# Kernel optimization log

Measured on AMD Instinct MI355X. Metric: run time of the kernel, lower is better.

Reference implementation:

```python
import jax, jax.numpy as jnp
import numpy as np

BS, Q, S1, S2 = 8, 128, 32, 64
H_DIM, NH = 768, 12
DH = H_DIM // NH


def _linear_params(k, scale=0.02):
    kw, _ = jax.random.split(k)
    w = jax.random.normal(kw, (H_DIM, H_DIM), jnp.float32) * scale
    b = jnp.zeros((H_DIM,), jnp.float32)
    return w, b


def setup_inputs() -> dict:
    root = jax.random.key(0)
    ks = jax.random.split(root, 12)
    wq_w, wq_b = _linear_params(ks[0])
    wk_w, wk_b = _linear_params(ks[1])
    wv_w, wv_b = _linear_params(ks[2])
    sq_w, sq_b = _linear_params(ks[3])
    sk_w, sk_b = _linear_params(ks[4])
    sv_w, sv_b = _linear_params(ks[5])
    return {
        "q_in": jax.random.normal(ks[6], (BS, Q, H_DIM), jnp.float32),
        "k_in": jax.random.normal(ks[7], (BS, S1, S2, H_DIM), jnp.float32),
        "v_in": jax.random.normal(ks[8], (BS, S1, S2, H_DIM), jnp.float32),
        "kvec": jax.random.normal(ks[9], (BS, S1, H_DIM), jnp.float32),
        "word_mask": jnp.ones((BS, S1, S2), jnp.int32),
        "sentence_mask": jnp.ones((BS * Q, S1), jnp.int32),
        "wq_w": wq_w, "wq_b": wq_b, "wk_w": wk_w, "wk_b": wk_b,
        "wv_w": wv_w, "wv_b": wv_b, "sq_w": sq_w, "sq_b": sq_b,
        "sk_w": sk_w, "sk_b": sk_b, "sv_w": sv_w, "sv_b": sv_b,
    }


def reference(q_in, k_in, v_in, kvec, word_mask, sentence_mask,
              wq_w, wq_b, wk_w, wk_b, wv_w, wv_b,
              sq_w, sq_b, sk_w, sk_b, sv_w, sv_b):
    bs, q_len = q_in.shape[0], q_in.shape[1]
    s1, s2 = k_in.shape[1], k_in.shape[2]
    scale = 1.0 / jnp.sqrt(jnp.float32(DH))

    # additive masks, as in the torch module
    wm = (1.0 - word_mask.astype(jnp.float32)) * -10000.0      # [bs, s1, s2]
    sm = (1.0 - sentence_mask.astype(jnp.float32)) * -10000.0  # [bs*Q, s1]

    # ---- word-level attention ----
    q = (q_in @ wq_w + wq_b).reshape(bs, q_len, NH, DH)
    k = (k_in @ wk_w + wk_b).reshape(bs, s1, s2, NH, DH)
    v = (v_in @ wv_w + wv_b).reshape(bs, s1, s2, NH, DH)
    # scores over tokens within each sentence: [bs, s1, H, Q, s2]
    scores1 = jnp.einsum('bqhd,bsthd->bshqt', q, k) * scale
    probs1 = jax.nn.softmax(scores1 + wm[:, :, None, None, :], axis=-1)
    # word_hidden: [bs, Q, s1, h]
    wh = jnp.einsum('bshqt,bsthd->bqshd', probs1, v).reshape(bs, q_len, s1, H_DIM)

    # ---- sentence-level attention ----
    sq = (q_in @ sq_w + sq_b).reshape(bs, q_len, NH, DH)
    sk = (kvec @ sk_w + sk_b).reshape(bs, s1, NH, DH)   # shared across queries
    sv = (wh @ sv_w + sv_b).reshape(bs, q_len, s1, NH, DH)
    scores2 = jnp.einsum('bqhd,bshd->bqhs', sq, sk) * scale  # [bs, Q, H, s1]
    scores2 = scores2 + sm.reshape(bs, q_len, s1)[:, :, None, :]
    probs2 = jax.nn.softmax(scores2, axis=-1)
    out = jnp.einsum('bqhs,bqshd->bqhd', probs2, sv).reshape(bs * q_len, H_DIM)
    return out
```

## Files before the change

kernel.cpp:

```cpp
#include <hip/hip_runtime.h>
#include <hip/hip_bf16.h>


typedef __attribute__((ext_vector_type(8))) short short8;
typedef __attribute__((ext_vector_type(4))) short short4v;
typedef __attribute__((ext_vector_type(4))) float f32x4;

__device__ __forceinline__ short f2bf(float f) {
  __hip_bfloat16 b = __float2bfloat16(f);
  return __builtin_bit_cast(short, b);
}
__device__ __forceinline__ float bf2f(short s) {
  __hip_bfloat16 b = __builtin_bit_cast(__hip_bfloat16, s);
  return __bfloat162float(b);
}

#define MFMA16(a, b, c) __builtin_amdgcn_mfma_f32_16x16x32_bf16((a), (b), (c), 0, 0, 0)

__device__ __forceinline__ void async_load16(const void* g, void* l) {
  auto l3 = (__attribute__((address_space(3))) void*)(uintptr_t)(
      reinterpret_cast<uintptr_t>(l));
  auto g1 = (const __attribute__((address_space(1))) void*)g;
  __builtin_amdgcn_global_load_lds(g1, l3, 16, 0, 0);
}

__global__ __launch_bounds__(256)
void prep(const float* __restrict__ w0, const float* __restrict__ w1,
          const float* __restrict__ w2, const float* __restrict__ w3,
          const float* __restrict__ w4, const float* __restrict__ w5,
          short* __restrict__ WT,
          const float* __restrict__ q_in, const float* __restrict__ k_in,
          const float* __restrict__ v_in, const float* __restrict__ kvec,
          short* __restrict__ qbf, short* __restrict__ kbf,
          short* __restrict__ vbf, short* __restrict__ kvb) {
  const int id = blockIdx.x;
  const int tid = threadIdx.x;
  if (id < 3456) {
    __shared__ float tile[32][33];
    const int zz = id / 576, r = id % 576;
    const float* W = (zz == 0) ? w0 : (zz == 1) ? w1 : (zz == 2) ? w2
                   : (zz == 3) ? w3 : (zz == 4) ? w4 : w5;
    short* WTo = WT + (size_t)zz * 768 * 768;
    const int bx = (r % 24) * 32, by = (r / 24) * 32;
    const int tx = tid & 31, ty = tid >> 5;
    #pragma unroll
    for (int i = 0; i < 32; i += 8)
      tile[ty + i][tx] = W[(size_t)(by + ty + i) * 768 + bx + tx];
    __syncthreads();
    #pragma unroll
    for (int i = 0; i < 32; i += 8)
      WTo[(size_t)(bx + ty + i) * 768 + by + tx] = f2bf(tile[tx][ty + i]);
    return;
  }
  const int i = (id - 3456) * 256 + tid;
  const float* src;
  short* dst;
  int idx;
  if (i < 98304)        { src = q_in; dst = qbf; idx = i; }
  else if (i < 1671168) { src = k_in; dst = kbf; idx = i - 98304; }
  else if (i < 3244032) { src = v_in; dst = vbf; idx = i - 1671168; }
  else                  { src = kvec; dst = kvb; idx = i - 3244032; }
  const float4* s = (const float4*)src + (size_t)idx * 2;
  const float4 a = s[0], b = s[1];
  __align__(16) short tmp[8] = {f2bf(a.x), f2bf(a.y), f2bf(a.z), f2bf(a.w),
                                f2bf(b.x), f2bf(b.y), f2bf(b.z), f2bf(b.w)};
  *((short8*)dst + idx) = *(short8*)tmp;
}

template<int OUT_MODE>
__global__ __launch_bounds__(256)
void gemm(const short* __restrict__ Ap, const short* __restrict__ Ap2,
          const short* __restrict__ WTa, const short* __restrict__ WTb,
          const float* __restrict__ bias_a, const float* __restrict__ bias_b,
          const float* __restrict__ probs2, void* __restrict__ Outp,
          void* __restrict__ Outp2) {
  const int K = 768;
  __shared__ __align__(16) short As[128 * 32];
  __shared__ __align__(16) short Bs[128 * 32];
  const int z = (OUT_MODE == 5) ? blockIdx.z : 0;
  const short* A = (OUT_MODE == 5 && z) ? Ap2 : Ap;
  const short* WT = (OUT_MODE == 5 && z) ? WTb : WTa;
  const float* bias = (OUT_MODE == 5 && z) ? bias_b : bias_a;

  const int tid = threadIdx.x;
  const int m0 = blockIdx.x * 128, n0 = blockIdx.y * 128;
  const int w = tid >> 6, lane = tid & 63, quad = lane >> 4, l16 = lane & 15;
  const int wm = (w >> 1) * 64, wn = (w & 1) * 64;

  const int grow = w * 32 + (lane >> 2);
  const int kc = (lane & 3) * 8;
  const short* ag = A + (size_t)(m0 + grow) * K + kc;
  const short* bg = WT + (size_t)(n0 + grow) * K + kc;
  short* al = &As[(w * 32) * 32];
  short* bl = &Bs[(w * 32) * 32];

  const f32x4 zero4 = {0.f, 0.f, 0.f, 0.f};
  f32x4 acc[4][4];
  #pragma unroll
  for (int i = 0; i < 4; i++)
    #pragma unroll
    for (int j = 0; j < 4; j++) acc[i][j] = zero4;

  for (int k0 = 0; k0 < K; k0 += 32) {
    __syncthreads();
    async_load16(ag, al);
    async_load16(ag + (size_t)16 * K, al + 16 * 32);
    async_load16(bg, bl);
    async_load16(bg + (size_t)16 * K, bl + 16 * 32);
    ag += 32;
    bg += 32;
    __syncthreads();
    short8 af[4], bf[4];
    #pragma unroll
    for (int i = 0; i < 4; i++)
      af[i] = *(short8*)&As[(wm + i * 16 + l16) * 32 + quad * 8];
    #pragma unroll
    for (int j = 0; j < 4; j++)
      bf[j] = *(short8*)&Bs[(wn + j * 16 + l16) * 32 + quad * 8];
    #pragma unroll
    for (int i = 0; i < 4; i++)
      #pragma unroll
      for (int j = 0; j < 4; j++)
        acc[i][j] = MFMA16(af[i], bf[j], acc[i][j]);
  }

  if (OUT_MODE == 4) {
    const int h = (n0 + wn) >> 6;
    const int bq0 = (m0 + wm) >> 5;
    float p2[2][2][4];
    #pragma unroll
    for (int g2 = 0; g2 < 2; g2++)
      #pragma unroll
      for (int par = 0; par < 2; par++)
        #pragma unroll
        for (int r = 0; r < 4; r++)
          p2[g2][par][r] =
              probs2[((size_t)(bq0 + g2) * 12 + h) * 32 + par * 16 + quad * 4 + r];
    float red[4][2];
    #pragma unroll
    for (int j = 0; j < 4; j++)
      #pragma unroll
      for (int g2 = 0; g2 < 2; g2++) {
        float ps = 0.f;
        #pragma unroll
        for (int par = 0; par < 2; par++)
          #pragma unroll
          for (int r = 0; r < 4; r++)
            ps += p2[g2][par][r] * acc[g2 * 2 + par][j][r];
        ps += __shfl_xor(ps, 16);
        ps += __shfl_xor(ps, 32);
        red[j][g2] = ps;
      }
    const int col = n0 + wn + quad * 16 + l16;
    const float bv = bias[col];
    float* outp = (float*)Outp;
    #pragma unroll
    for (int g2 = 0; g2 < 2; g2++)
      outp[(size_t)(bq0 + g2) * 768 + col] = red[quad][g2] + bv;
    return;
  }

  if (OUT_MODE == 5 && z == 1) {
    const int bs_ = (m0 + wm) >> 6;
    const int hh = (n0 + wn) >> 6;
    short* vT = (short*)Outp2;
    #pragma unroll
    for (int i = 0; i < 4; i++) {
      const int t0 = i * 16 + quad * 4;
      #pragma unroll
      for (int j = 0; j < 4; j++) {
        const int dd = j * 16 + l16;
        const float bv = bias[hh * 64 + dd];
        __align__(8) short tmp[4];
        #pragma unroll
        for (int r = 0; r < 4; r++) tmp[r] = f2bf(acc[i][j][r] + bv);
        *(short4v*)&vT[(((size_t)bs_ * 12 + hh) * 64 + dd) * 64 + t0] = *(short4v*)tmp;
      }
    }
    return;
  }

  #pragma unroll
  for (int i = 0; i < 4; i++) {
    #pragma unroll
    for (int j = 0; j < 4; j++) {
      const int col = n0 + wn + j * 16 + l16;
      float bv;
      if (OUT_MODE == 3)
        bv = (col < 768) ? bias_a[col] : bias_b[col - 768];
      else
        bv = bias[col];
      #pragma unroll
      for (int r = 0; r < 4; r++) {
        const int g = m0 + wm + i * 16 + quad * 4 + r;
        const float v = acc[i][j][r] + bv;
        if (OUT_MODE == 0) {
          ((float*)Outp)[(size_t)g * 768 + col] = v;
        } else if (OUT_MODE == 5) {
          ((short*)Outp)[(size_t)g * 768 + col] = f2bf(v);
        } else {
          if (col < 768)
            ((short*)Outp)[(size_t)g * 768 + col] = f2bf(v * 0.125f);
          else
            ((float*)Outp2)[(size_t)g * 768 + (col - 768)] = v;
        }
      }
    }
  }
}

__global__ __launch_bounds__(256)
void wattn_sp(const short* __restrict__ q_proj, const short* __restrict__ k_proj,
              const short* __restrict__ vT, const int* __restrict__ word_mask,
              const float* __restrict__ sq, const float* __restrict__ sk,
              const int* __restrict__ sent_mask, short* __restrict__ wh,
              float* __restrict__ probs2) {
  __shared__ __align__(16) short KVs[128 * 72];
  __shared__ __align__(16) short Ps[128 * 72];
  const int bid = blockIdx.x;
  const int tid = threadIdx.x;

  if (bid >= 3072) {
    float* sc = (float*)KVs;
    const int bq = bid - 3072;
    const int b = bq >> 7, q = bq & 127;
    for (int p = tid; p < 384; p += 256) {
      const int hh = p >> 5, ss = p & 31;
      const float4* a = (const float4*)(sq + ((size_t)(b * 128 + q)) * 768 + hh * 64);
      const float4* c = (const float4*)(sk + ((size_t)(b * 32 + ss)) * 768 + hh * 64);
      float d = 0.f;
      #pragma unroll
      for (int i = 0; i < 16; i++) {
        const float4 av = a[i], cv = c[i];
        d += av.x * cv.x + av.y * cv.y + av.z * cv.z + av.w * cv.w;
      }
      d = d * 0.125f + (1.0f - (float)sent_mask[bq * 32 + ss]) * -10000.0f;
      sc[hh * 33 + ss] = d;
    }
    __syncthreads();
    if (tid < 12) {
      float mx = -3.0e38f;
      for (int ss = 0; ss < 32; ss++) mx = fmaxf(mx, sc[tid * 33 + ss]);
      float sum = 0.f;
      for (int ss = 0; ss < 32; ss++) {
        const float e = __expf(sc[tid * 33 + ss] - mx);
        sc[tid * 33 + ss] = e;
        sum += e;
      }
      const float inv = 1.0f / sum;
      for (int ss = 0; ss < 32; ss++) sc[tid * 33 + ss] *= inv;
    }
    __syncthreads();
    for (int p = tid; p < 384; p += 256) {
      const int hh = p >> 5, ss = p & 31;
      probs2[((size_t)bq * 12 + hh) * 32 + ss] = sc[hh * 33 + ss];
    }
    return;
  }

  short* Ks = KVs;
  short* Vs = KVs + 64 * 72;
  short* Os = KVs;
  const int h = bid % 12, s = (bid / 12) % 32, b = bid / (12 * 32);
  const int w = tid >> 6, lane = tid & 63, quad = lane >> 4, l16 = lane & 15;
  const f32x4 zero4 = {0.f, 0.f, 0.f, 0.f};

  {
    const int t2 = tid & 127;
    const int row8 = t2 >> 3;
    const int c8 = (t2 & 7) * 8;
    if (tid < 128) {
      const short* src = k_proj + ((size_t)((b * 32 + s) * 64)) * 768 + h * 64 + c8;
      #pragma unroll
      for (int i = 0; i < 4; i++) {
        const int r = row8 + i * 16;
        *(short8*)&Ks[r * 72 + c8] = *(const short8*)(src + (size_t)r * 768);
      }
    } else {
      const short* src = vT + ((size_t)((b * 32 + s) * 12 + h)) * 4096 + c8;
      #pragma unroll
      for (int i = 0; i < 4; i++) {
        const int r = row8 + i * 16;
        *(short8*)&Vs[r * 72 + c8] = *(const short8*)(src + (size_t)r * 64);
      }
    }
  }
  __syncthreads();

  f32x4 sac[2][4];
  #pragma unroll
  for (int i = 0; i < 2; i++)
    #pragma unroll
    for (int j = 0; j < 4; j++) sac[i][j] = zero4;
  {
    short8 aq[2][2], bk[4][2];
    #pragma unroll
    for (int i = 0; i < 2; i++)
      #pragma unroll
      for (int kb = 0; kb < 2; kb++)
        aq[i][kb] = *(const short8*)(q_proj +
            ((size_t)(b * 128 + w * 32 + i * 16 + l16)) * 768 + h * 64 + kb * 32 + quad * 8);
    #pragma unroll
    for (int j = 0; j < 4; j++)
      #pragma unroll
      for (int kb = 0; kb < 2; kb++)
        bk[j][kb] = *(short8*)&Ks[(j * 16 + l16) * 72 + kb * 32 + quad * 8];
    #pragma unroll
    for (int i = 0; i < 2; i++)
      #pragma unroll
      for (int j = 0; j < 4; j++) {
        sac[i][j] = MFMA16(aq[i][0], bk[j][0], sac[i][j]);
        sac[i][j] = MFMA16(aq[i][1], bk[j][1], sac[i][j]);
      }
  }

  {
    float wmv[4];
    const int* wmp = word_mask + (b * 32 + s) * 64;
    #pragma unroll
    for (int j = 0; j < 4; j++)
      wmv[j] = (1.0f - (float)wmp[j * 16 + l16]) * -10000.0f;
    #pragma unroll
    for (int i = 0; i < 2; i++) {
      #pragma unroll
      for (int r = 0; r < 4; r++) {
        float vv[4];
        float sum = 0.f;
        #pragma unroll
        for (int j = 0; j < 4; j++) {
          vv[j] = __expf(sac[i][j][r] + wmv[j]);
          sum += vv[j];
        }
        sum += __shfl_xor(sum, 1);
        sum += __shfl_xor(sum, 2);
        sum += __shfl_xor(sum, 4);
        sum += __shfl_xor(sum, 8);
        const float inv = 1.0f / sum;
        const int row = w * 32 + i * 16 + quad * 4 + r;
        #pragma unroll
        for (int j = 0; j < 4; j++)
          Ps[row * 72 + j * 16 + l16] = f2bf(vv[j] * inv);
      }
    }
  }
  __syncthreads();

  f32x4 oac[2][4];
  #pragma unroll
  for (int i = 0; i < 2; i++)
    #pragma unroll
    for (int j = 0; j < 4; j++) oac[i][j] = zero4;
  {
    short8 ap[2][2], bv[4][2];
    #pragma unroll
    for (int i = 0; i < 2; i++)
      #pragma unroll
      for (int kb = 0; kb < 2; kb++)
        ap[i][kb] = *(short8*)&Ps[(w * 32 + i * 16 + l16) * 72 + kb * 32 + quad * 8];
    #pragma unroll
    for (int j = 0; j < 4; j++)
      #pragma unroll
      for (int kb = 0; kb < 2; kb++)
        bv[j][kb] = *(short8*)&Vs[(j * 16 + l16) * 72 + kb * 32 + quad * 8];
    #pragma unroll
    for (int i = 0; i < 2; i++)
      #pragma unroll
      for (int j = 0; j < 4; j++) {
        oac[i][j] = MFMA16(ap[i][0], bv[j][0], oac[i][j]);
        oac[i][j] = MFMA16(ap[i][1], bv[j][1], oac[i][j]);
      }
  }
  __syncthreads();
  #pragma unroll
  for (int i = 0; i < 2; i++)
    #pragma unroll
    for (int j = 0; j < 4; j++)
      #pragma unroll
      for (int r = 0; r < 4; r++)
        Os[(w * 32 + i * 16 + quad * 4 + r) * 72 + j * 16 + l16] = f2bf(oac[i][j][r]);
  __syncthreads();

  {
    const int c8 = (tid & 7) * 8;
    #pragma unroll
    for (int i = 0; i < 4; i++) {
      const int row = i * 32 + (tid >> 3);
      short* dst = wh + (((size_t)(b * 128 + row)) * 32 + s) * 768 + h * 64;
      *(short8*)(dst + c8) = *(const short8*)&Os[row * 72 + c8];
    }
  }
}

extern "C" void kernel_launch(void* const* d_in, const int* in_sizes, int n_in,
                              void* d_out, int out_size, void* d_ws, size_t ws_size,
                              hipStream_t stream) {
  (void)in_sizes; (void)n_in; (void)out_size; (void)ws_size;
  const float* q_in      = (const float*)d_in[0];
  const float* k_in      = (const float*)d_in[1];
  const float* v_in      = (const float*)d_in[2];
  const float* kvec      = (const float*)d_in[3];
  const int*   word_mask = (const int*)d_in[4];
  const int*   sent_mask = (const int*)d_in[5];
  const float* wq_w = (const float*)d_in[6],  *wq_b = (const float*)d_in[7];
  const float* wk_w = (const float*)d_in[8],  *wk_b = (const float*)d_in[9];
  const float* wv_w = (const float*)d_in[10], *wv_b = (const float*)d_in[11];
  const float* sq_w = (const float*)d_in[12], *sq_b = (const float*)d_in[13];
  const float* sk_w = (const float*)d_in[14], *sk_b = (const float*)d_in[15];
  const float* sv_w = (const float*)d_in[16], *sv_b = (const float*)d_in[17];
  float* out = (float*)d_out;

  char* ws = (char*)d_ws;
  size_t off = 0;
  auto alloc = [&](size_t bytes) -> void* {
    void* p = ws + off;
    off += (bytes + 255) & ~(size_t)255;
    return p;
  };
  short* WT  = (short*)alloc((size_t)6 * 768 * 768 * 2);
  short* qbf = (short*)alloc((size_t)1024 * 768 * 2);
  short* kbf = (short*)alloc((size_t)16384 * 768 * 2);
  short* vbf = (short*)alloc((size_t)16384 * 768 * 2);
  short* kvb = (short*)alloc((size_t)256 * 768 * 2);
  short* qp  = (short*)alloc((size_t)1024 * 768 * 2);
  short* kp  = (short*)alloc((size_t)16384 * 768 * 2);
  short* vT  = (short*)alloc((size_t)16384 * 768 * 2);
  float* sqp = (float*)alloc((size_t)1024 * 768 * 4);
  float* skp = (float*)alloc((size_t)256 * 768 * 4);
  short* wh  = (short*)alloc((size_t)32768 * 768 * 2);
  float* pr2 = (float*)alloc((size_t)1024 * 12 * 32 * 4);

  const int WELEM = 768 * 768;

  prep<<<dim3(16224), 256, 0, stream>>>(wq_w, sq_w, wk_w, wv_w, sk_w, sv_w, WT,
                                        q_in, k_in, v_in, kvec, qbf, kbf, vbf, kvb);
  gemm<3><<<dim3(8, 12), 256, 0, stream>>>(qbf, nullptr, WT + 0 * WELEM, nullptr,
                                           wq_b, sq_b, nullptr, qp, sqp);
  gemm<5><<<dim3(128, 6, 2), 256, 0, stream>>>(kbf, vbf, WT + 2 * WELEM, WT + 3 * WELEM,
                                               wk_b, wv_b, nullptr, kp, vT);
  gemm<0><<<dim3(2, 6), 256, 0, stream>>>(kvb, nullptr, WT + 4 * WELEM, nullptr,
                                          sk_b, nullptr, nullptr, skp, nullptr);
  wattn_sp<<<dim3(4096), 256, 0, stream>>>(qp, kp, vT, word_mask, sqp, skp,
                                           sent_mask, wh, pr2);
  gemm<4><<<dim3(256, 6), 256, 0, stream>>>(wh, nullptr, WT + 5 * WELEM, nullptr,
                                            sv_b, nullptr, pr2, out, nullptr);
}
```

Baseline: 360.9 us.

## Contract sentence probs before sv projection and merge projection GEMMs into one launch

The final stage no longer projects every word-hidden row through sv_w and then reduces with the sentence probabilities. A new kernel first forms per-head probability-weighted sums of wh over sentences. A smaller per-head GEMM then applies the matching 64 columns of sv_w plus the bias, which removes most of the large output-projection FLOPs. The three input projection GEMMs (q/sq, k/v, kvec) are also folded into one launch with block-id-based dispatch. In exchange there is an extra bf16 intermediate buffer, a scalar FMA reduction kernel, and a low-block-count final GEMM.

```diff
diff --git a/kernel.cpp b/kernel.cpp
--- a/kernel.cpp
+++ b/kernel.cpp
@@ -67,23 +67,31 @@
   *((short8*)dst + idx) = *(short8*)tmp;
 }
 
-template<int OUT_MODE>
 __global__ __launch_bounds__(256)
-void gemm(const short* __restrict__ Ap, const short* __restrict__ Ap2,
-          const short* __restrict__ WTa, const short* __restrict__ WTb,
-          const float* __restrict__ bias_a, const float* __restrict__ bias_b,
-          const float* __restrict__ probs2, void* __restrict__ Outp,
-          void* __restrict__ Outp2) {
-  const int K = 768;
+void proj_all(const short* __restrict__ qbf, const short* __restrict__ kbf,
+              const short* __restrict__ vbf, const short* __restrict__ kvb,
+              const short* __restrict__ WT6,
+              const float* __restrict__ wq_b, const float* __restrict__ sq_b,
+              const float* __restrict__ wk_b, const float* __restrict__ wv_b,
+              const float* __restrict__ sk_b,
+              short* __restrict__ qp, float* __restrict__ sqp,
+              short* __restrict__ kp, short* __restrict__ vT,
+              float* __restrict__ skp) {
+  const int K = 768, WELEM = 768 * 768;
   __shared__ __align__(16) short As[128 * 32];
   __shared__ __align__(16) short Bs[128 * 32];
-  const int z = (OUT_MODE == 5) ? blockIdx.z : 0;
-  const short* A = (OUT_MODE == 5 && z) ? Ap2 : Ap;
-  const short* WT = (OUT_MODE == 5 && z) ? WTb : WTa;
-  const float* bias = (OUT_MODE == 5 && z) ? bias_b : bias_a;
+
+  const int id = blockIdx.x;
+  int mode, bx, by;
+  const short* A;
+  const short* WT;
+  if (id < 768)       { mode = 0; bx = id % 128;  by = id / 128;  A = kbf; WT = WT6 + 2 * WELEM; }
+  else if (id < 1536) { mode = 1; const int r = id - 768;  bx = r % 128; by = r / 128; A = vbf; WT = WT6 + 3 * WELEM; }
+  else if (id < 1632) { mode = 2; const int r = id - 1536; bx = r % 8;   by = r / 8;   A = qbf; WT = WT6 + 0 * WELEM; }
+  else                { mode = 3; const int r = id - 1632; bx = r % 2;   by = r / 2;   A = kvb; WT = WT6 + 4 * WELEM; }
 
   const int tid = threadIdx.x;
-  const int m0 = blockIdx.x * 128, n0 = blockIdx.y * 128;
+  const int m0 = bx * 128, n0 = by * 128;
   const int w = tid >> 6, lane = tid & 63, quad = lane >> 4, l16 = lane & 15;
   const int wm = (w >> 1) * 64, wn = (w & 1) * 64;
 
@@ -124,53 +132,16 @@
         acc[i][j] = MFMA16(af[i], bf[j], acc[i][j]);
   }
 
-  if (OUT_MODE == 4) {
-    const int h = (n0 + wn) >> 6;
-    const int bq0 = (m0 + wm) >> 5;
-    float p2[2][2][4];
-    #pragma unroll
-    for (int g2 = 0; g2 < 2; g2++)
-      #pragma unroll
-      for (int par = 0; par < 2; par++)
-        #pragma unroll
-        for (int r = 0; r < 4; r++)
-          p2[g2][par][r] =
-              probs2[((size_t)(bq0 + g2) * 12 + h) * 32 + par * 16 + quad * 4 + r];
-    float red[4][2];
-    #pragma unroll
-    for (int j = 0; j < 4; j++)
-      #pragma unroll
-      for (int g2 = 0; g2 < 2; g2++) {
-        float ps = 0.f;
-        #pragma unroll
-        for (int par = 0; par < 2; par++)
-          #pragma unroll
-          for (int r = 0; r < 4; r++)
-            ps += p2[g2][par][r] * acc[g2 * 2 + par][j][r];
-        ps += __shfl_xor(ps, 16);
-        ps += __shfl_xor(ps, 32);
-        red[j][g2] = ps;
-      }
-    const int col = n0 + wn + quad * 16 + l16;
-    const float bv = bias[col];
-    float* outp = (float*)Outp;
-    #pragma unroll
-    for (int g2 = 0; g2 < 2; g2++)
-      outp[(size_t)(bq0 + g2) * 768 + col] = red[quad][g2] + bv;
-    return;
-  }
-
-  if (OUT_MODE == 5 && z == 1) {
+  if (mode == 1) {
     const int bs_ = (m0 + wm) >> 6;
     const int hh = (n0 + wn) >> 6;
-    short* vT = (short*)Outp2;
     #pragma unroll
     for (int i = 0; i < 4; i++) {
       const int t0 = i * 16 + quad * 4;
       #pragma unroll
       for (int j = 0; j < 4; j++) {
         const int dd = j * 16 + l16;
-        const float bv = bias[hh * 64 + dd];
+        const float bv = wv_b[hh * 64 + dd];
         __align__(8) short tmp[4];
         #pragma unroll
         for (int r = 0; r < 4; r++) tmp[r] = f2bf(acc[i][j][r] + bv);
@@ -179,30 +150,26 @@
     }
     return;
   }
-
   #pragma unroll
   for (int i = 0; i < 4; i++) {
     #pragma unroll
     for (int j = 0; j < 4; j++) {
       const int col = n0 + wn + j * 16 + l16;
       float bv;
-      if (OUT_MODE == 3)
-        bv = (col < 768) ? bias_a[col] : bias_b[col - 768];
-      else
-        bv = bias[col];
+      if (mode == 0) bv = wk_b[col];
+      else if (mode == 2) bv = (col < 768) ? wq_b[col] : sq_b[col - 768];
+      else bv = sk_b[col];
       #pragma unroll
       for (int r = 0; r < 4; r++) {
         const int g = m0 + wm + i * 16 + quad * 4 + r;
         const float v = acc[i][j][r] + bv;
-        if (OUT_MODE == 0) {
-          ((float*)Outp)[(size_t)g * 768 + col] = v;
-        } else if (OUT_MODE == 5) {
-          ((short*)Outp)[(size_t)g * 768 + col] = f2bf(v);
+        if (mode == 0) {
+          kp[(size_t)g * 768 + col] = f2bf(v);
+        } else if (mode == 2) {
+          if (col < 768) qp[(size_t)g * 768 + col] = f2bf(v * 0.125f);
+          else sqp[(size_t)g * 768 + (col - 768)] = v;
         } else {
-          if (col < 768)
-            ((short*)Outp)[(size_t)g * 768 + col] = f2bf(v * 0.125f);
-          else
-            ((float*)Outp2)[(size_t)g * 768 + (col - 768)] = v;
+          skp[(size_t)g * 768 + col] = v;
         }
       }
     }
@@ -387,6 +354,107 @@
       const int row = i * 32 + (tid >> 3);
       short* dst = wh + (((size_t)(b * 128 + row)) * 32 + s) * 768 + h * 64;
       *(short8*)(dst + c8) = *(const short8*)&Os[row * 72 + c8];
+    }
+  }
+}
+
+__global__ __launch_bounds__(256)
+void whc_kernel(const short* __restrict__ wh, const float* __restrict__ probs2,
+                short* __restrict__ whc) {
+  __shared__ __align__(16) short whs[32 * 776];
+  __shared__ float p2s[384];
+  const int bq = blockIdx.x, tid = threadIdx.x;
+  const short8* src = (const short8*)(wh + (size_t)bq * 24576);
+  for (int t = tid; t < 3072; t += 256) {
+    const int row = t / 96, c8 = (t % 96) * 8;
+    *(short8*)&whs[row * 776 + c8] = src[t];
+  }
+  for (int p = tid; p < 384; p += 256) p2s[p] = probs2[(size_t)bq * 384 + p];
+  __syncthreads();
+
+  float acc[3][12];
+  #pragma unroll
+  for (int kk = 0; kk < 3; kk++)
+    #pragma unroll
+    for (int h = 0; h < 12; h++) acc[kk][h] = 0.f;
+
+  for (int s = 0; s < 32; s++) {
+    float p2r[12];
+    #pragma unroll
+    for (int h = 0; h < 12; h++) p2r[h] = p2s[h * 32 + s];
+    #pragma unroll
+    for (int kk = 0; kk < 3; kk++) {
+      const float wv = bf2f(whs[s * 776 + kk * 256 + tid]);
+      #pragma unroll
+      for (int h = 0; h < 12; h++) acc[kk][h] += p2r[h] * wv;
+    }
+  }
+  #pragma unroll
+  for (int h = 0; h < 12; h++)
+    #pragma unroll
+    for (int kk = 0; kk < 3; kk++)
+      whc[((size_t)h * 1024 + bq) * 768 + kk * 256 + tid] = f2bf(acc[kk][h]);
+}
+
+__global__ __launch_bounds__(256)
+void outg(const short* __restrict__ whc, const short* __restrict__ WTsv,
+          const float* __restrict__ sv_b, float* __restrict__ out) {
+  const int K = 768;
+  __shared__ __align__(16) short As[128 * 32];
+  __shared__ __align__(16) short Bs[64 * 32];
+  const int tid = threadIdx.x;
+  const int m0 = blockIdx.x * 128, h = blockIdx.y;
+  const int w = tid >> 6, lane = tid & 63, quad = lane >> 4, l16 = lane & 15;
+  const int wm = (w >> 1) * 64, wn = (w & 1) * 32;
+
+  const int grow = w * 32 + (lane >> 2);
+  const int kc = (lane & 3) * 8;
+  const short* ag = whc + ((size_t)h * 1024 + m0 + grow) * K + kc;
+  short* al = &As[(w * 32) * 32];
+  const int growb = w * 16 + (lane >> 2);
+  const short* bg = WTsv + (size_t)(h * 64 + growb) * K + kc;
+  short* bl = &Bs[(w * 16) * 32];
+
+  const f32x4 zero4 = {0.f, 0.f, 0.f, 0.f};
+  f32x4 acc[4][2];
+  #pragma unroll
+  for (int i = 0; i < 4; i++)
+    #pragma unroll
+    for (int j = 0; j < 2; j++) acc[i][j] = zero4;
+
+  for (int k0 = 0; k0 < K; k0 += 32) {
+    __syncthreads();
+    async_load16(ag, al);
+    async_load16(ag + (size_t)16 * K, al + 16 * 32);
+    async_load16(bg, bl);
+    ag += 32;
+    bg += 32;
+    __syncthreads();
+    short8 af[4], bf[2];
+    #pragma unroll
+    for (int i = 0; i < 4; i++)
+      af[i] = *(short8*)&As[(wm + i * 16 + l16) * 32 + quad * 8];
+    #pragma unroll
+    for (int j = 0; j < 2; j++)
+      bf[j] = *(short8*)&Bs[(wn + j * 16 + l16) * 32 + quad * 8];
+    #pragma unroll
+    for (int i = 0; i < 4; i++)
+      #pragma unroll
+      for (int j = 0; j < 2; j++)
+        acc[i][j] = MFMA16(af[i], bf[j], acc[i][j]);
+  }
+
+  #pragma unroll
+  for (int i = 0; i < 4; i++) {
+    #pragma unroll
+    for (int j = 0; j < 2; j++) {
+      const int col = h * 64 + wn + j * 16 + l16;
+      const float bv = sv_b[col];
+      #pragma unroll
+      for (int r = 0; r < 4; r++) {
+        const int g = m0 + wm + i * 16 + quad * 4 + r;
+        out[(size_t)g * 768 + col] = acc[i][j][r] + bv;
+      }
     }
   }
 }
@@ -428,19 +496,17 @@
   float* skp = (float*)alloc((size_t)256 * 768 * 4);
   short* wh  = (short*)alloc((size_t)32768 * 768 * 2);
   float* pr2 = (float*)alloc((size_t)1024 * 12 * 32 * 4);
+  short* whc = (short*)alloc((size_t)12 * 1024 * 768 * 2);
 
   const int WELEM = 768 * 768;
 
   prep<<<dim3(16224), 256, 0, stream>>>(wq_w, sq_w, wk_w, wv_w, sk_w, sv_w, WT,
                                         q_in, k_in, v_in, kvec, qbf, kbf, vbf, kvb);
-  gemm<3><<<dim3(8, 12), 256, 0, stream>>>(qbf, nullptr, WT + 0 * WELEM, nullptr,
-                                           wq_b, sq_b, nullptr, qp, sqp);
-  gemm<5><<<dim3(128, 6, 2), 256, 0, stream>>>(kbf, vbf, WT + 2 * WELEM, WT + 3 * WELEM,
-                                               wk_b, wv_b, nullptr, kp, vT);
-  gemm<0><<<dim3(2, 6), 256, 0, stream>>>(kvb, nullptr, WT + 4 * WELEM, nullptr,
-                                          sk_b, nullptr, nullptr, skp, nullptr);
+  proj_all<<<dim3(1644), 256, 0, stream>>>(qbf, kbf, vbf, kvb, WT,
+                                           wq_b, sq_b, wk_b, wv_b, sk_b,
+                                           qp, sqp, kp, vT, skp);
   wattn_sp<<<dim3(4096), 256, 0, stream>>>(qp, kp, vT, word_mask, sqp, skp,
                                            sent_mask, wh, pr2);
-  gemm<4><<<dim3(256, 6), 256, 0, stream>>>(wh, nullptr, WT + 5 * WELEM, nullptr,
-                                            sv_b, nullptr, pr2, out, nullptr);
-}
+  whc_kernel<<<dim3(1024), 256, 0, stream>>>(wh, pr2, whc);
+  outg<<<dim3(8, 12), 256, 0, stream>>>(whc, WT + 5 * WELEM, sv_b, out);
+}
```

After: 345.5 us. 4.3% less time.
